# Kernel optimization log

Measured on AMD Instinct MI355X. Metric: run time of the kernel, lower is better.

## Reference

```python
import jax, jax.numpy as jnp
import numpy as np

N_NODES = 100000
N_EDGES = 1600000
IN_DIM = 64
OUT_DIM = 64
HIDDEN = 64  # fixed in edge_weight_mlp
POS_DIM = 3


def setup_inputs() -> dict:
    key = jax.random.key(0)
    ks = jax.random.split(key, 10)
    x = jax.random.normal(ks[0], (N_NODES, IN_DIM), dtype=jnp.float32)
    edge_index = jax.random.randint(ks[1], (2, N_EDGES), 0, N_NODES, dtype=jnp.int64)
    pos = jax.random.normal(ks[2], (N_NODES, POS_DIM), dtype=jnp.float32)
    # edge_weight_mlp params: Linear(2*IN_DIM+1 -> 64), Linear(64 -> 1)
    s1 = 1.0 / np.sqrt(2 * IN_DIM + 1)
    w1 = jax.random.uniform(ks[3], (2 * IN_DIM + 1, HIDDEN), jnp.float32, -s1, s1)
    b1 = jax.random.uniform(ks[4], (HIDDEN,), jnp.float32, -s1, s1)
    s2 = 1.0 / np.sqrt(HIDDEN)
    w2 = jax.random.uniform(ks[5], (HIDDEN, 1), jnp.float32, -s2, s2)
    b2 = jax.random.uniform(ks[6], (1,), jnp.float32, -s2, s2)
    # transform: Linear(IN_DIM -> OUT_DIM)
    st = 1.0 / np.sqrt(IN_DIM)
    wt = jax.random.uniform(ks[7], (IN_DIM, OUT_DIM), jnp.float32, -st, st)
    bt = jax.random.uniform(ks[8], (OUT_DIM,), jnp.float32, -st, st)
    return {"x": x, "edge_index": edge_index, "pos": pos,
            "w1": w1, "b1": b1, "w2": w2, "b2": b2, "wt": wt, "bt": bt}


def reference(x, edge_index, pos, w1, b1, w2, b2, wt, bt):
    src, dst = edge_index[0], edge_index[1]
    # edge weights: MLP on [x_src, x_dst, |pos_dst - pos_src|]
    edge_length = jnp.linalg.norm(pos[dst] - pos[src], axis=1, keepdims=True)  # [E,1]
    edge_feat = jnp.concatenate([x[src], x[dst], edge_length], axis=1)  # [E, 2*in+1]
    h = jax.nn.relu(edge_feat @ w1 + b1)
    edge_weights = jax.nn.sigmoid(h @ w2 + b2)  # [E,1]
    # node transform, gather, weight, scatter-add
    x_t = x @ wt + bt  # [N, out]
    messages = x_t[src] * edge_weights  # [E, out]
    out = jax.ops.segment_sum(messages, dst, num_segments=x.shape[0])  # [N, out]
    return out, edge_weights
```

## Files before the change

kernel.cpp:

```cpp
#include <hip/hip_runtime.h>
#include <hip/hip_bf16.h>
#include <math.h>

#define NN 100000
#define NE 1600000
#define CAP 48
#define NB 391
#define BCAP 4608
#define EPB 4096
#define NBLKA ((NE + EPB - 1) / EPB)
#define NPREP ((NN + 63) / 64)
#define PSTR 72

typedef __attribute__((ext_vector_type(8))) short short8;
typedef __attribute__((ext_vector_type(4))) float floatx4;
typedef __attribute__((ext_vector_type(2))) float float2v;

#if __has_builtin(__builtin_elementwise_fma)
#define VFMA(a, b, c) __builtin_elementwise_fma((a), (b), (c))
#else
#define VFMA(a, b, c) ((a) * (b) + (c))
#endif

static __device__ __forceinline__ unsigned short f2bb(float f) {
    __hip_bfloat16 h = __float2bfloat16(f);
    return *(unsigned short*)&h;
}
static __device__ __forceinline__ float hi_f(unsigned u) {
    return __uint_as_float(u & 0xFFFF0000u);
}
static __device__ __forceinline__ float lo_f(unsigned u) {
    return __uint_as_float(u << 16);
}
static __device__ __forceinline__ float2v hi2(unsigned a, unsigned b) {
    float2v r; r.x = __uint_as_float(a & 0xFFFF0000u);
    r.y = __uint_as_float(b & 0xFFFF0000u); return r;
}
static __device__ __forceinline__ float2v lo2(unsigned a, unsigned b) {
    float2v r; r.x = __uint_as_float(a << 16);
    r.y = __uint_as_float(b << 16); return r;
}

__global__ __launch_bounds__(256) void init_kernel(
    const float* __restrict__ w1, const float* __restrict__ wt,
    unsigned short* __restrict__ wb, int* __restrict__ gcursor) {
    int t = threadIdx.x;
    if (blockIdx.x == 0) {
        for (int i = t; i < NB; i += 256) gcursor[i] = 0;
    }
    int stride = gridDim.x * 256;
    for (int idx = blockIdx.x * 256 + t; idx < 192 * 64; idx += stride) {
        int n = idx >> 6;
        int k = idx & 63;
        float v = (n < 64)  ? w1[(size_t)k * 64 + n]
                : (n < 128) ? w1[(size_t)(64 + k) * 64 + (n - 64)]
                            : wt[(size_t)k * 64 + (n - 128)];
        wb[idx] = f2bb(v);
    }
}

__global__ __launch_bounds__(256) void fused_prep_bucket(
    const float* __restrict__ x, const unsigned short* __restrict__ wb,
    const float* __restrict__ b1, const float* __restrict__ pos,
    const int* __restrict__ ei,
    unsigned int* __restrict__ rec, unsigned short* __restrict__ hd,
    float4* __restrict__ pos4, int* __restrict__ gcursor,
    uint2* __restrict__ bucketed) {
    __shared__ __align__(16) unsigned char smem[(64 + 192) * PSTR * 2];
    int t = threadIdx.x;
    if (blockIdx.x < NPREP) {
        unsigned short* As = (unsigned short*)smem;
        unsigned short* Bs = As + 64 * PSTR;
        int nbase = blockIdx.x * 64;
        {
            int r = t & 63;
            int node = nbase + r; if (node >= NN) node = NN - 1;
            const float4* xr = (const float4*)(x + (size_t)node * 64);
#pragma unroll
            for (int i = 0; i < 4; ++i) {
                int s = (t >> 6) + 4 * i;
                float4 v = xr[s];
                ushort4 o = {f2bb(v.x), f2bb(v.y), f2bb(v.z), f2bb(v.w)};
                *(ushort4*)&As[r * PSTR + s * 4] = o;
            }
        }
        {
            const uint4* wb4 = (const uint4*)wb;
#pragma unroll
            for (int i = 0; i < 6; ++i) {
                int v = t + 256 * i;
                uint4 q = wb4[v];
                int n = v >> 3;
                int k = (v & 7) * 8;
                *(uint4*)&Bs[n * PSTR + k] = q;
            }
        }
        if (t < 64) {
            int node = nbase + t;
            if (node < NN)
                pos4[node] = make_float4(pos[node * 3 + 0], pos[node * 3 + 1],
                                         pos[node * 3 + 2], 0.f);
        }
        __syncthreads();
        int lane = t & 63, wave = t >> 6;
        int grp = lane >> 4, l15 = lane & 15;
        floatx4 acc[12] = {};
        int arow = wave * 16 + l15;
#pragma unroll
        for (int ks = 0; ks < 2; ++ks) {
            int koff = ks * 32 + grp * 8;
            short8 a = *(const short8*)&As[arow * PSTR + koff];
#pragma unroll
            for (int nt = 0; nt < 12; ++nt) {
                short8 b = *(const short8*)&Bs[(nt * 16 + l15) * PSTR + koff];
                acc[nt] = __builtin_amdgcn_mfma_f32_16x16x32_bf16(a, b, acc[nt], 0, 0, 0);
            }
        }
#pragma unroll
        for (int nt = 0; nt < 4; ++nt) {
#pragma unroll
            for (int r = 0; r < 4; ++r) {
                int nr = wave * 16 + grp * 4 + r;
                int node = nbase + nr;
                if (node >= NN) continue;
                int col = nt * 16 + l15;
                rec[(size_t)node * 64 + col] =
                    ((unsigned)f2bb(acc[nt][r]) << 16) | f2bb(acc[8 + nt][r]);
                hd[(size_t)node * 64 + col] = f2bb(acc[4 + nt][r] + b1[col]);
            }
        }
    } else {
        int* cnt = (int*)smem;
        int* base_s = cnt + NB;
        for (int i = t; i < NB; i += 256) cnt[i] = 0;
        __syncthreads();
        int e0 = (blockIdx.x - NPREP) * EPB;
        unsigned int tags[16];
        int srcs[16], dsts[16];
#pragma unroll
        for (int i = 0; i < 16; ++i) {
            int e = e0 + i * 256 + t;
            tags[i] = 0xFFFFFFFFu;
            if (e < NE) {
                srcs[i] = ei[e];
                dsts[i] = ei[NE + e];
                int b = dsts[i] >> 8;
                int slot = atomicAdd(&cnt[b], 1);
                tags[i] = ((unsigned)b << 12) | (unsigned)slot;
            }
        }
        __syncthreads();
        for (int b = t; b < NB; b += 256)
            base_s[b] = atomicAdd(&gcursor[b], cnt[b]);
        __syncthreads();
#pragma unroll
        for (int i = 0; i < 16; ++i) {
            if (tags[i] != 0xFFFFFFFFu) {
                int e = e0 + i * 256 + t;
                int b = (int)(tags[i] >> 12);
                int slot = (int)(tags[i] & 0xFFFu);
                int p = base_s[b] + slot;
                if (p < BCAP) {
                    bucketed[(size_t)b * BCAP + p] =
                        make_uint2((unsigned)srcs[i] |
                                   (((unsigned)dsts[i] & 255u) << 17),
                                   (unsigned)e);
                }
            }
        }
    }
}

__global__ __launch_bounds__(1024) void csr_kernel(
    const uint2* __restrict__ bucketed, const int* __restrict__ gcursor,
    uint2* __restrict__ pairs, int* __restrict__ deg) {
    __shared__ int cur[256];
    int t = threadIdx.x;
    if (t < 256) cur[t] = 0;
    __syncthreads();
    int b = blockIdx.x;
    int n0 = b << 8;
    int cnt = gcursor[b];
    if (cnt > BCAP) cnt = BCAP;
    for (int i = t; i < cnt; i += 1024) {
        uint2 en = bucketed[(size_t)b * BCAP + i];
        int dwb = (int)((en.x >> 17) & 255u);
        unsigned src = en.x & 0x1FFFFu;
        int slot = atomicAdd(&cur[dwb], 1);
        if (slot < CAP)
            pairs[(size_t)(n0 + dwb) * CAP + slot] = make_uint2(src, en.y);
    }
    __syncthreads();
    if (t < 256) {
        int node = n0 + t;
        if (node < NN) deg[node] = (cur[t] > CAP) ? CAP : cur[t];
    }
}

__global__ __launch_bounds__(256) void mega_kernel(
    const uint2* __restrict__ pairs, const int* __restrict__ deg,
    const unsigned int* __restrict__ rec, const unsigned short* __restrict__ hd,
    const float4* __restrict__ pos4, const float* __restrict__ w1,
    const float* __restrict__ w2, const float* __restrict__ b2,
    const float* __restrict__ bt,
    float* __restrict__ ew_out, float* __restrict__ out) {
    int t = threadIdx.x;
    int w = t >> 6, lane = t & 63;
    int e8 = lane >> 3, hg = lane & 7;
    int node = blockIdx.x * 4 + w;
    if (node >= NN) return;

    const float2v zero2 = {0.f, 0.f};
    float2v a01 = zero2, a23 = zero2, a45 = zero2, a67 = zero2;
    float sw = 0.f;
    int d = deg[node];
    uint4 hz = ((const uint4*)(hd + (size_t)node * 64))[hg];
    float2v zb01 = {lo_f(hz.x), hi_f(hz.x)};
    float2v zb23 = {lo_f(hz.y), hi_f(hz.y)};
    float2v zb45 = {lo_f(hz.z), hi_f(hz.z)};
    float2v zb67 = {lo_f(hz.w), hi_f(hz.w)};
    const float2v* w2p = (const float2v*)(w2 + 8 * hg);
    float2v w20 = w2p[0], w21 = w2p[1], w22 = w2p[2], w23 = w2p[3];
    const float2v* wlp = (const float2v*)(w1 + 128 * 64 + 8 * hg);
    float2v wl0 = wlp[0], wl1 = wlp[1], wl2 = wlp[2], wl3 = wlp[3];
    float4 bta = ((const float4*)bt)[2 * hg];
    float4 btb = ((const float4*)bt)[2 * hg + 1];
    float4 pd = pos4[node];
    float b2v = b2[0];
    const uint2* seg = pairs + (size_t)node * CAP;
    const uint4* rec4 = (const uint4*)rec;

    if (d > 0) {
        int i0 = (e8 < d) ? e8 : (d - 1);
        uint2 pr_c = seg[i0];
        uint2 pr_n = pr_c;
        if (8 < d) { int i1 = (8 + e8 < d) ? (8 + e8) : (d - 1); pr_n = seg[i1]; }
        uint4 ua_c = rec4[(size_t)pr_c.x * 16 + 2 * hg];
        uint4 ub_c = rec4[(size_t)pr_c.x * 16 + 2 * hg + 1];
        float4 ps_c = pos4[pr_c.x];

#pragma unroll 2
        for (int j = 0; j < d; j += 8) {
            int jn = j + 8;
            uint2 pr_n2 = pr_n;
            uint4 ua_n = ua_c, ub_n = ub_c;
            float4 ps_n = ps_c;
            if (jn < d) {
                ua_n = rec4[(size_t)pr_n.x * 16 + 2 * hg];
                ub_n = rec4[(size_t)pr_n.x * 16 + 2 * hg + 1];
                ps_n = pos4[pr_n.x];
                if (jn + 8 < d) {
                    int i2 = (jn + 8 + e8 < d) ? (jn + 8 + e8) : (d - 1);
                    pr_n2 = seg[i2];
                }
            }
            bool valid = (j + e8 < d);
            float dx = pd.x - ps_c.x;
            float dy = pd.y - ps_c.y;
            float dz = pd.z - ps_c.z;
            float len = __builtin_amdgcn_sqrtf(dx * dx + dy * dy + dz * dz);
            float2v l2; l2.x = len; l2.y = len;
            float2v z, r, tp;
            z = zb01 + hi2(ua_c.x, ua_c.y); z = VFMA(l2, wl0, z);
            r = __builtin_elementwise_max(z, zero2); tp = r * w20;
            z = zb23 + hi2(ua_c.z, ua_c.w); z = VFMA(l2, wl1, z);
            r = __builtin_elementwise_max(z, zero2); tp = VFMA(r, w21, tp);
            z = zb45 + hi2(ub_c.x, ub_c.y); z = VFMA(l2, wl2, z);
            r = __builtin_elementwise_max(z, zero2); tp = VFMA(r, w22, tp);
            z = zb67 + hi2(ub_c.z, ub_c.w); z = VFMA(l2, wl3, z);
            r = __builtin_elementwise_max(z, zero2); tp = VFMA(r, w23, tp);
            float tt = tp.x + tp.y;
            tt += __shfl_xor(tt, 1);
            tt += __shfl_xor(tt, 2);
            tt += __shfl_xor(tt, 4);
            float ew = __builtin_amdgcn_rcpf(1.f + __expf(-(tt + b2v)));
            if (valid) {
                if (hg == 0) ew_out[pr_c.y] = ew;
                float2v e2; e2.x = ew; e2.y = ew;
                a01 = VFMA(e2, lo2(ua_c.x, ua_c.y), a01);
                a23 = VFMA(e2, lo2(ua_c.z, ua_c.w), a23);
                a45 = VFMA(e2, lo2(ub_c.x, ub_c.y), a45);
                a67 = VFMA(e2, lo2(ub_c.z, ub_c.w), a67);
                sw += ew;
            }
            pr_c = pr_n; pr_n = pr_n2;
            ua_c = ua_n; ub_c = ub_n; ps_c = ps_n;
        }
    }
    float acc0 = a01.x, acc1 = a01.y, acc2 = a23.x, acc3 = a23.y;
    float acc4 = a45.x, acc5 = a45.y, acc6 = a67.x, acc7 = a67.y;
#pragma unroll
    for (int off = 8; off < 64; off <<= 1) {
        acc0 += __shfl_xor(acc0, off);
        acc1 += __shfl_xor(acc1, off);
        acc2 += __shfl_xor(acc2, off);
        acc3 += __shfl_xor(acc3, off);
        acc4 += __shfl_xor(acc4, off);
        acc5 += __shfl_xor(acc5, off);
        acc6 += __shfl_xor(acc6, off);
        acc7 += __shfl_xor(acc7, off);
        sw   += __shfl_xor(sw, off);
    }
    if (e8 == 0) {
        float* orow = out + (size_t)node * 64 + hg * 8;
        float4 o1 = {acc0 + sw * bta.x, acc1 + sw * bta.y,
                     acc2 + sw * bta.z, acc3 + sw * bta.w};
        float4 o2 = {acc4 + sw * btb.x, acc5 + sw * btb.y,
                     acc6 + sw * btb.z, acc7 + sw * btb.w};
        *(float4*)orow = o1;
        *(float4*)(orow + 4) = o2;
    }
}

extern "C" void kernel_launch(void* const* d_in, const int* in_sizes, int n_in,
                              void* d_out, int out_size, void* d_ws, size_t ws_size,
                              hipStream_t stream) {
    const float* x   = (const float*)d_in[0];
    const int*   ei  = (const int*)d_in[1];
    const float* pos = (const float*)d_in[2];
    const float* w1  = (const float*)d_in[3];
    const float* b1  = (const float*)d_in[4];
    const float* w2  = (const float*)d_in[5];
    const float* b2  = (const float*)d_in[6];
    const float* wt  = (const float*)d_in[7];
    const float* bt  = (const float*)d_in[8];

    float* out    = (float*)d_out;
    float* ew_out = out + (size_t)NN * 64;

    unsigned int* rec = (unsigned int*)d_ws;
    unsigned short* hd = (unsigned short*)(rec + (size_t)NN * 64);
    uint2* pairs = (uint2*)(hd + (size_t)NN * 64);
    float4* pos4 = (float4*)(pairs + (size_t)NN * CAP);
    int* gcursor = (int*)(pos4 + NN);
    int* deg = gcursor + NB;
    unsigned short* wb = (unsigned short*)(deg + NN);

    uint2* bucketed = (uint2*)d_out;

    init_kernel<<<16, 256, 0, stream>>>(w1, wt, wb, gcursor);
    fused_prep_bucket<<<NPREP + NBLKA, 256, 0, stream>>>(
        x, wb, b1, pos, ei, rec, hd, pos4, gcursor, bucketed);
    csr_kernel<<<NB, 1024, 0, stream>>>(bucketed, gcursor, pairs, deg);
    mega_kernel<<<(NN + 3) / 4, 256, 0, stream>>>(pairs, deg, rec, hd, pos4,
                                                  w1, w2, b2, bt, ew_out, out);
}
```

Before: 236.6 us.

## Stage bucketed edges in LDS via prefix scan for coalesced global writes

Both the bucketing pass and the CSR build now sort entries locally in shared memory using a block-wide prefix scan over bucket counts. They then write to global memory in contiguous runs instead of scattered per-entry stores. The aim is to cut uncoalesced scatter traffic in both passes. The cost is a larger LDS footprint, which may lower occupancy, plus extra scan steps and barriers. The per-thread register staging in csr_kernel assumes at most 5 entries per thread.

```diff
diff --git a/kernel.cpp b/kernel.cpp
--- a/kernel.cpp
+++ b/kernel.cpp
@@ -66,7 +66,7 @@
     unsigned int* __restrict__ rec, unsigned short* __restrict__ hd,
     float4* __restrict__ pos4, int* __restrict__ gcursor,
     uint2* __restrict__ bucketed) {
-    __shared__ __align__(16) unsigned char smem[(64 + 192) * PSTR * 2];
+    __shared__ __align__(16) unsigned char smem[40960];
     int t = threadIdx.x;
     if (blockIdx.x < NPREP) {
         unsigned short* As = (unsigned short*)smem;
@@ -130,9 +130,12 @@
             }
         }
     } else {
-        int* cnt = (int*)smem;
-        int* base_s = cnt + NB;
-        for (int i = t; i < NB; i += 256) cnt[i] = 0;
+        uint2* staged = (uint2*)smem;
+        int* cnt = (int*)(staged + EPB);
+        int* scA = cnt + 512;
+        int* scB = scA + 512;
+        int* base_s = scB + 512;
+        for (int i = t; i < 512; i += 256) cnt[i] = 0;
         __syncthreads();
         int e0 = (blockIdx.x - NPREP) * EPB;
         unsigned int tags[16];
@@ -150,23 +153,38 @@
             }
         }
         __syncthreads();
+        for (int i = t; i < 512; i += 256) scA[i] = cnt[i];
+        __syncthreads();
+        int* sp = scA; int* dp = scB;
+        for (int off = 1; off < 512; off <<= 1) {
+            for (int i = t; i < 512; i += 256)
+                dp[i] = sp[i] + ((i >= off) ? sp[i - off] : 0);
+            __syncthreads();
+            int* tmp = sp; sp = dp; dp = tmp;
+        }
         for (int b = t; b < NB; b += 256)
             base_s[b] = atomicAdd(&gcursor[b], cnt[b]);
-        __syncthreads();
 #pragma unroll
         for (int i = 0; i < 16; ++i) {
             if (tags[i] != 0xFFFFFFFFu) {
                 int e = e0 + i * 256 + t;
                 int b = (int)(tags[i] >> 12);
                 int slot = (int)(tags[i] & 0xFFFu);
-                int p = base_s[b] + slot;
-                if (p < BCAP) {
-                    bucketed[(size_t)b * BCAP + p] =
-                        make_uint2((unsigned)srcs[i] |
-                                   (((unsigned)dsts[i] & 255u) << 17),
-                                   (unsigned)e);
-                }
-            }
+                int pos = sp[b] - cnt[b] + slot;
+                staged[pos] = make_uint2(
+                    (unsigned)srcs[i] | (((unsigned)dsts[i] & 255u) << 17),
+                    (unsigned)e | ((unsigned)b << 21));
+            }
+        }
+        __syncthreads();
+        int total = sp[511];
+        for (int i = t; i < total; i += 256) {
+            uint2 en = staged[i];
+            int b = (int)(en.y >> 21);
+            int p = base_s[b] + (i - (sp[b] - cnt[b]));
+            if (p < BCAP)
+                bucketed[(size_t)b * BCAP + p] =
+                    make_uint2(en.x, en.y & 0x1FFFFFu);
         }
     }
 }
@@ -174,7 +192,8 @@
 __global__ __launch_bounds__(1024) void csr_kernel(
     const uint2* __restrict__ bucketed, const int* __restrict__ gcursor,
     uint2* __restrict__ pairs, int* __restrict__ deg) {
-    __shared__ int cur[256];
+    __shared__ uint2 staged[BCAP];
+    __shared__ int cur[256], scA[256], scB[256];
     int t = threadIdx.x;
     if (t < 256) cur[t] = 0;
     __syncthreads();
@@ -182,13 +201,41 @@
     int n0 = b << 8;
     int cnt = gcursor[b];
     if (cnt > BCAP) cnt = BCAP;
+    uint2 en_r[5];
+    int slot_r[5];
+    int k = 0;
     for (int i = t; i < cnt; i += 1024) {
         uint2 en = bucketed[(size_t)b * BCAP + i];
         int dwb = (int)((en.x >> 17) & 255u);
-        unsigned src = en.x & 0x1FFFFu;
-        int slot = atomicAdd(&cur[dwb], 1);
-        if (slot < CAP)
-            pairs[(size_t)(n0 + dwb) * CAP + slot] = make_uint2(src, en.y);
+        slot_r[k] = atomicAdd(&cur[dwb], 1);
+        en_r[k] = en;
+        ++k;
+    }
+    __syncthreads();
+    if (t < 256) scA[t] = cur[t];
+    __syncthreads();
+    int* sp = scA; int* dp = scB;
+    for (int off = 1; off < 256; off <<= 1) {
+        if (t < 256) dp[t] = sp[t] + ((t >= off) ? sp[t - off] : 0);
+        __syncthreads();
+        int* tmp = sp; sp = dp; dp = tmp;
+    }
+    k = 0;
+    for (int i = t; i < cnt; i += 1024) {
+        uint2 en = en_r[k];
+        int dwb = (int)((en.x >> 17) & 255u);
+        int pos = sp[dwb] - cur[dwb] + slot_r[k];
+        staged[pos] = en;
+        ++k;
+    }
+    __syncthreads();
+    for (int i = t; i < cnt; i += 1024) {
+        uint2 en = staged[i];
+        int dwb = (int)((en.x >> 17) & 255u);
+        int p = i - (sp[dwb] - cur[dwb]);
+        if (p < CAP)
+            pairs[(size_t)(n0 + dwb) * CAP + p] =
+                make_uint2(en.x & 0x1FFFFu, en.y);
     }
     __syncthreads();
     if (t < 256) {
```

After: 252.7 us. 6.8% more time.

## Fuse CSR build into gather kernel using LDS-staged per-bucket edge lists

Applied to the files above, without the earlier changes.

Removes the separate csr_kernel and its global pairs/deg arrays. Each 1024-thread block now loads its bucket of edges, counts per-destination slots with LDS atomics, prefix-sums the counts and scatters the edges into shared memory. The same block then runs the per-node edge MLP and aggregation from LDS, which saves a launch and a global write and read of the CSR. The cost is only NB=391 large blocks (about 37KB of LDS each), so fewer blocks run concurrently and there is less latency hiding for the gathers. The bucket buffer also moves from the output to the workspace, and the degree cap of 48 per node is gone.

```diff
diff --git a/kernel.cpp b/kernel.cpp
--- a/kernel.cpp
+++ b/kernel.cpp
@@ -4,7 +4,6 @@
 
 #define NN 100000
 #define NE 1600000
-#define CAP 48
 #define NB 391
 #define BCAP 4608
 #define EPB 4096
@@ -171,144 +170,157 @@
     }
 }
 
-__global__ __launch_bounds__(1024) void csr_kernel(
+__global__ __launch_bounds__(1024) void mega_kernel(
     const uint2* __restrict__ bucketed, const int* __restrict__ gcursor,
-    uint2* __restrict__ pairs, int* __restrict__ deg) {
-    __shared__ int cur[256];
-    int t = threadIdx.x;
-    if (t < 256) cur[t] = 0;
-    __syncthreads();
-    int b = blockIdx.x;
-    int n0 = b << 8;
-    int cnt = gcursor[b];
-    if (cnt > BCAP) cnt = BCAP;
-    for (int i = t; i < cnt; i += 1024) {
-        uint2 en = bucketed[(size_t)b * BCAP + i];
-        int dwb = (int)((en.x >> 17) & 255u);
-        unsigned src = en.x & 0x1FFFFu;
-        int slot = atomicAdd(&cur[dwb], 1);
-        if (slot < CAP)
-            pairs[(size_t)(n0 + dwb) * CAP + slot] = make_uint2(src, en.y);
-    }
-    __syncthreads();
-    if (t < 256) {
-        int node = n0 + t;
-        if (node < NN) deg[node] = (cur[t] > CAP) ? CAP : cur[t];
-    }
-}
-
-__global__ __launch_bounds__(256) void mega_kernel(
-    const uint2* __restrict__ pairs, const int* __restrict__ deg,
     const unsigned int* __restrict__ rec, const unsigned short* __restrict__ hd,
     const float4* __restrict__ pos4, const float* __restrict__ w1,
     const float* __restrict__ w2, const float* __restrict__ b2,
     const float* __restrict__ bt,
     float* __restrict__ ew_out, float* __restrict__ out) {
+    __shared__ uint2 staged[BCAP];
+    __shared__ int cur[256], scA[256], scB[256], off_s[256];
     int t = threadIdx.x;
+    int b = blockIdx.x;
+    int n0 = b << 8;
+    if (t < 256) cur[t] = 0;
+    __syncthreads();
+    int cnt = gcursor[b];
+    if (cnt > BCAP) cnt = BCAP;
+    uint2 en_r[5];
+    int slot_r[5];
+    int k = 0;
+    for (int i = t; i < cnt; i += 1024) {
+        uint2 en = bucketed[(size_t)b * BCAP + i];
+        int dwb = (int)((en.x >> 17) & 255u);
+        slot_r[k] = atomicAdd(&cur[dwb], 1);
+        en_r[k] = en;
+        ++k;
+    }
+    __syncthreads();
+    if (t < 256) scA[t] = cur[t];
+    __syncthreads();
+    int* sp = scA; int* dp = scB;
+    for (int off = 1; off < 256; off <<= 1) {
+        if (t < 256) dp[t] = sp[t] + ((t >= off) ? sp[t - off] : 0);
+        __syncthreads();
+        int* tmp = sp; sp = dp; dp = tmp;
+    }
+    if (t < 256) off_s[t] = sp[t] - cur[t];
+    __syncthreads();
+    k = 0;
+    for (int i = t; i < cnt; i += 1024) {
+        uint2 en = en_r[k];
+        int dwb = (int)((en.x >> 17) & 255u);
+        staged[off_s[dwb] + slot_r[k]] = en;
+        ++k;
+    }
+    __syncthreads();
+
     int w = t >> 6, lane = t & 63;
     int e8 = lane >> 3, hg = lane & 7;
-    int node = blockIdx.x * 4 + w;
-    if (node >= NN) return;
-
     const float2v zero2 = {0.f, 0.f};
-    float2v a01 = zero2, a23 = zero2, a45 = zero2, a67 = zero2;
-    float sw = 0.f;
-    int d = deg[node];
-    uint4 hz = ((const uint4*)(hd + (size_t)node * 64))[hg];
-    float2v zb01 = {lo_f(hz.x), hi_f(hz.x)};
-    float2v zb23 = {lo_f(hz.y), hi_f(hz.y)};
-    float2v zb45 = {lo_f(hz.z), hi_f(hz.z)};
-    float2v zb67 = {lo_f(hz.w), hi_f(hz.w)};
     const float2v* w2p = (const float2v*)(w2 + 8 * hg);
     float2v w20 = w2p[0], w21 = w2p[1], w22 = w2p[2], w23 = w2p[3];
     const float2v* wlp = (const float2v*)(w1 + 128 * 64 + 8 * hg);
     float2v wl0 = wlp[0], wl1 = wlp[1], wl2 = wlp[2], wl3 = wlp[3];
     float4 bta = ((const float4*)bt)[2 * hg];
     float4 btb = ((const float4*)bt)[2 * hg + 1];
-    float4 pd = pos4[node];
     float b2v = b2[0];
-    const uint2* seg = pairs + (size_t)node * CAP;
     const uint4* rec4 = (const uint4*)rec;
 
-    if (d > 0) {
-        int i0 = (e8 < d) ? e8 : (d - 1);
-        uint2 pr_c = seg[i0];
-        uint2 pr_n = pr_c;
-        if (8 < d) { int i1 = (8 + e8 < d) ? (8 + e8) : (d - 1); pr_n = seg[i1]; }
-        uint4 ua_c = rec4[(size_t)pr_c.x * 16 + 2 * hg];
-        uint4 ub_c = rec4[(size_t)pr_c.x * 16 + 2 * hg + 1];
-        float4 ps_c = pos4[pr_c.x];
+    for (int ni = 0; ni < 16; ++ni) {
+        int local = w * 16 + ni;
+        int node = n0 + local;
+        if (node >= NN) break;
+        float2v a01 = zero2, a23 = zero2, a45 = zero2, a67 = zero2;
+        float sw = 0.f;
+        int d = cur[local];
+        int so = off_s[local];
+        uint4 hz = ((const uint4*)(hd + (size_t)node * 64))[hg];
+        float2v zb01 = {lo_f(hz.x), hi_f(hz.x)};
+        float2v zb23 = {lo_f(hz.y), hi_f(hz.y)};
+        float2v zb45 = {lo_f(hz.z), hi_f(hz.z)};
+        float2v zb67 = {lo_f(hz.w), hi_f(hz.w)};
+        float4 pd = pos4[node];
+
+        if (d > 0) {
+            int i0 = (e8 < d) ? e8 : (d - 1);
+            uint2 pr_c = staged[so + i0];
+            unsigned s_c = pr_c.x & 0x1FFFFu;
+            uint4 ua_c = rec4[(size_t)s_c * 16 + 2 * hg];
+            uint4 ub_c = rec4[(size_t)s_c * 16 + 2 * hg + 1];
+            float4 ps_c = pos4[s_c];
 
 #pragma unroll 2
-        for (int j = 0; j < d; j += 8) {
-            int jn = j + 8;
-            uint2 pr_n2 = pr_n;
-            uint4 ua_n = ua_c, ub_n = ub_c;
-            float4 ps_n = ps_c;
-            if (jn < d) {
-                ua_n = rec4[(size_t)pr_n.x * 16 + 2 * hg];
-                ub_n = rec4[(size_t)pr_n.x * 16 + 2 * hg + 1];
-                ps_n = pos4[pr_n.x];
-                if (jn + 8 < d) {
-                    int i2 = (jn + 8 + e8 < d) ? (jn + 8 + e8) : (d - 1);
-                    pr_n2 = seg[i2];
+            for (int j = 0; j < d; j += 8) {
+                int jn = j + 8;
+                uint2 pr_n = pr_c;
+                uint4 ua_n = ua_c, ub_n = ub_c;
+                float4 ps_n = ps_c;
+                if (jn < d) {
+                    int i1 = (jn + e8 < d) ? (jn + e8) : (d - 1);
+                    pr_n = staged[so + i1];
+                    unsigned s_n = pr_n.x & 0x1FFFFu;
+                    ua_n = rec4[(size_t)s_n * 16 + 2 * hg];
+                    ub_n = rec4[(size_t)s_n * 16 + 2 * hg + 1];
+                    ps_n = pos4[s_n];
                 }
-            }
-            bool valid = (j + e8 < d);
-            float dx = pd.x - ps_c.x;
-            float dy = pd.y - ps_c.y;
-            float dz = pd.z - ps_c.z;
-            float len = __builtin_amdgcn_sqrtf(dx * dx + dy * dy + dz * dz);
-            float2v l2; l2.x = len; l2.y = len;
-            float2v z, r, tp;
-            z = zb01 + hi2(ua_c.x, ua_c.y); z = VFMA(l2, wl0, z);
-            r = __builtin_elementwise_max(z, zero2); tp = r * w20;
-            z = zb23 + hi2(ua_c.z, ua_c.w); z = VFMA(l2, wl1, z);
-            r = __builtin_elementwise_max(z, zero2); tp = VFMA(r, w21, tp);
-            z = zb45 + hi2(ub_c.x, ub_c.y); z = VFMA(l2, wl2, z);
-            r = __builtin_elementwise_max(z, zero2); tp = VFMA(r, w22, tp);
-            z = zb67 + hi2(ub_c.z, ub_c.w); z = VFMA(l2, wl3, z);
-            r = __builtin_elementwise_max(z, zero2); tp = VFMA(r, w23, tp);
-            float tt = tp.x + tp.y;
-            tt += __shfl_xor(tt, 1);
-            tt += __shfl_xor(tt, 2);
-            tt += __shfl_xor(tt, 4);
-            float ew = __builtin_amdgcn_rcpf(1.f + __expf(-(tt + b2v)));
-            if (valid) {
-                if (hg == 0) ew_out[pr_c.y] = ew;
-                float2v e2; e2.x = ew; e2.y = ew;
-                a01 = VFMA(e2, lo2(ua_c.x, ua_c.y), a01);
-                a23 = VFMA(e2, lo2(ua_c.z, ua_c.w), a23);
-                a45 = VFMA(e2, lo2(ub_c.x, ub_c.y), a45);
-                a67 = VFMA(e2, lo2(ub_c.z, ub_c.w), a67);
-                sw += ew;
-            }
-            pr_c = pr_n; pr_n = pr_n2;
-            ua_c = ua_n; ub_c = ub_n; ps_c = ps_n;
-        }
-    }
-    float acc0 = a01.x, acc1 = a01.y, acc2 = a23.x, acc3 = a23.y;
-    float acc4 = a45.x, acc5 = a45.y, acc6 = a67.x, acc7 = a67.y;
-#pragma unroll
-    for (int off = 8; off < 64; off <<= 1) {
-        acc0 += __shfl_xor(acc0, off);
-        acc1 += __shfl_xor(acc1, off);
-        acc2 += __shfl_xor(acc2, off);
-        acc3 += __shfl_xor(acc3, off);
-        acc4 += __shfl_xor(acc4, off);
-        acc5 += __shfl_xor(acc5, off);
-        acc6 += __shfl_xor(acc6, off);
-        acc7 += __shfl_xor(acc7, off);
-        sw   += __shfl_xor(sw, off);
-    }
-    if (e8 == 0) {
-        float* orow = out + (size_t)node * 64 + hg * 8;
-        float4 o1 = {acc0 + sw * bta.x, acc1 + sw * bta.y,
-                     acc2 + sw * bta.z, acc3 + sw * bta.w};
-        float4 o2 = {acc4 + sw * btb.x, acc5 + sw * btb.y,
-                     acc6 + sw * btb.z, acc7 + sw * btb.w};
-        *(float4*)orow = o1;
-        *(float4*)(orow + 4) = o2;
+                bool valid = (j + e8 < d);
+                float dx = pd.x - ps_c.x;
+                float dy = pd.y - ps_c.y;
+                float dz = pd.z - ps_c.z;
+                float len = __builtin_amdgcn_sqrtf(dx * dx + dy * dy + dz * dz);
+                float2v l2; l2.x = len; l2.y = len;
+                float2v z, r, tp;
+                z = zb01 + hi2(ua_c.x, ua_c.y); z = VFMA(l2, wl0, z);
+                r = __builtin_elementwise_max(z, zero2); tp = r * w20;
+                z = zb23 + hi2(ua_c.z, ua_c.w); z = VFMA(l2, wl1, z);
+                r = __builtin_elementwise_max(z, zero2); tp = VFMA(r, w21, tp);
+                z = zb45 + hi2(ub_c.x, ub_c.y); z = VFMA(l2, wl2, z);
+                r = __builtin_elementwise_max(z, zero2); tp = VFMA(r, w22, tp);
+                z = zb67 + hi2(ub_c.z, ub_c.w); z = VFMA(l2, wl3, z);
+                r = __builtin_elementwise_max(z, zero2); tp = VFMA(r, w23, tp);
+                float tt = tp.x + tp.y;
+                tt += __shfl_xor(tt, 1);
+                tt += __shfl_xor(tt, 2);
+                tt += __shfl_xor(tt, 4);
+                float ew = __builtin_amdgcn_rcpf(1.f + __expf(-(tt + b2v)));
+                if (valid) {
+                    if (hg == 0) ew_out[pr_c.y] = ew;
+                    float2v e2; e2.x = ew; e2.y = ew;
+                    a01 = VFMA(e2, lo2(ua_c.x, ua_c.y), a01);
+                    a23 = VFMA(e2, lo2(ua_c.z, ua_c.w), a23);
+                    a45 = VFMA(e2, lo2(ub_c.x, ub_c.y), a45);
+                    a67 = VFMA(e2, lo2(ub_c.z, ub_c.w), a67);
+                    sw += ew;
+                }
+                pr_c = pr_n;
+                ua_c = ua_n; ub_c = ub_n; ps_c = ps_n;
+            }
+        }
+        float acc0 = a01.x, acc1 = a01.y, acc2 = a23.x, acc3 = a23.y;
+        float acc4 = a45.x, acc5 = a45.y, acc6 = a67.x, acc7 = a67.y;
+#pragma unroll
+        for (int off = 8; off < 64; off <<= 1) {
+            acc0 += __shfl_xor(acc0, off);
+            acc1 += __shfl_xor(acc1, off);
+            acc2 += __shfl_xor(acc2, off);
+            acc3 += __shfl_xor(acc3, off);
+            acc4 += __shfl_xor(acc4, off);
+            acc5 += __shfl_xor(acc5, off);
+            acc6 += __shfl_xor(acc6, off);
+            acc7 += __shfl_xor(acc7, off);
+            sw   += __shfl_xor(sw, off);
+        }
+        if (e8 == 0) {
+            float* orow = out + (size_t)node * 64 + hg * 8;
+            float4 o1 = {acc0 + sw * bta.x, acc1 + sw * bta.y,
+                         acc2 + sw * bta.z, acc3 + sw * bta.w};
+            float4 o2 = {acc4 + sw * btb.x, acc5 + sw * btb.y,
+                         acc6 + sw * btb.z, acc7 + sw * btb.w};
+            *(float4*)orow = o1;
+            *(float4*)(orow + 4) = o2;
+        }
     }
 }
 
@@ -330,18 +342,14 @@
 
     unsigned int* rec = (unsigned int*)d_ws;
     unsigned short* hd = (unsigned short*)(rec + (size_t)NN * 64);
-    uint2* pairs = (uint2*)(hd + (size_t)NN * 64);
-    float4* pos4 = (float4*)(pairs + (size_t)NN * CAP);
+    uint2* bucketed = (uint2*)(hd + (size_t)NN * 64);
+    float4* pos4 = (float4*)(bucketed + (size_t)NB * BCAP);
     int* gcursor = (int*)(pos4 + NN);
-    int* deg = gcursor + NB;
-    unsigned short* wb = (unsigned short*)(deg + NN);
-
-    uint2* bucketed = (uint2*)d_out;
+    unsigned short* wb = (unsigned short*)(gcursor + NB);
 
     init_kernel<<<16, 256, 0, stream>>>(w1, wt, wb, gcursor);
     fused_prep_bucket<<<NPREP + NBLKA, 256, 0, stream>>>(
         x, wb, b1, pos, ei, rec, hd, pos4, gcursor, bucketed);
-    csr_kernel<<<NB, 1024, 0, stream>>>(bucketed, gcursor, pairs, deg);
-    mega_kernel<<<(NN + 3) / 4, 256, 0, stream>>>(pairs, deg, rec, hd, pos4,
-                                                  w1, w2, b2, bt, ew_out, out);
-}
+    mega_kernel<<<NB, 1024, 0, stream>>>(bucketed, gcursor, rec, hd, pos4,
+                                         w1, w2, b2, bt, ew_out, out);
+}
```

Measured after the change: 250.9 us. 6.0% more time.

## Split fused prep/bucket kernel into separate launches with larger prep tiles

Applied to the files above, without the earlier changes.

Undoes the fusion of node-transform GEMM blocks and edge-bucketing blocks into one launch, and issues them as two kernels on the same stream. The prep kernel now uses 512 threads covering 128 nodes per block, which halves the number of times each block stages the weight matrix into shared memory. It also uses packed bf16 conversion instructions and hoists the bias load out of the inner loop. The cost is one extra kernel launch and the loss of any overlap between the two heterogeneous block types.

```diff
diff --git a/kernel.cpp b/kernel.cpp
--- a/kernel.cpp
+++ b/kernel.cpp
@@ -9,7 +9,7 @@
 #define BCAP 4608
 #define EPB 4096
 #define NBLKA ((NE + EPB - 1) / EPB)
-#define NPREP ((NN + 63) / 64)
+#define NPREP2 ((NN + 127) / 128)
 #define PSTR 72
 
 typedef __attribute__((ext_vector_type(8))) short short8;
@@ -25,6 +25,11 @@
 static __device__ __forceinline__ unsigned short f2bb(float f) {
     __hip_bfloat16 h = __float2bfloat16(f);
     return *(unsigned short*)&h;
+}
+static __device__ __forceinline__ unsigned cvt_pk_bf16(float lo, float hi) {
+    unsigned r;
+    asm("v_cvt_pk_bf16_f32 %0, %1, %2" : "=v"(r) : "v"(lo), "v"(hi));
+    return r;
 }
 static __device__ __forceinline__ float hi_f(unsigned u) {
     return __uint_as_float(u & 0xFFFF0000u);
@@ -59,113 +64,114 @@
     }
 }
 
-__global__ __launch_bounds__(256) void fused_prep_bucket(
+__global__ __launch_bounds__(512) void prep_kernel(
     const float* __restrict__ x, const unsigned short* __restrict__ wb,
     const float* __restrict__ b1, const float* __restrict__ pos,
-    const int* __restrict__ ei,
     unsigned int* __restrict__ rec, unsigned short* __restrict__ hd,
-    float4* __restrict__ pos4, int* __restrict__ gcursor,
+    float4* __restrict__ pos4) {
+    __shared__ __align__(16) unsigned short As[128 * PSTR];
+    __shared__ __align__(16) unsigned short Bs[192 * PSTR];
+    int t = threadIdx.x;
+    int nbase = blockIdx.x * 128;
+    {
+        int r = t & 127;
+        int node = nbase + r; if (node >= NN) node = NN - 1;
+        const float4* xr = (const float4*)(x + (size_t)node * 64);
+#pragma unroll
+        for (int i = 0; i < 4; ++i) {
+            int s = (t >> 7) + 4 * i;
+            float4 v = xr[s];
+            *(uint2*)&As[r * PSTR + s * 4] =
+                make_uint2(cvt_pk_bf16(v.x, v.y), cvt_pk_bf16(v.z, v.w));
+        }
+    }
+    {
+        const uint4* wb4 = (const uint4*)wb;
+#pragma unroll
+        for (int i = 0; i < 3; ++i) {
+            int v = t + 512 * i;
+            uint4 q = wb4[v];
+            int n = v >> 3;
+            int k = (v & 7) * 8;
+            *(uint4*)&Bs[n * PSTR + k] = q;
+        }
+    }
+    if (t < 128) {
+        int node = nbase + t;
+        if (node < NN)
+            pos4[node] = make_float4(pos[node * 3 + 0], pos[node * 3 + 1],
+                                     pos[node * 3 + 2], 0.f);
+    }
+    __syncthreads();
+    int lane = t & 63, wave = t >> 6;
+    int grp = lane >> 4, l15 = lane & 15;
+    floatx4 acc[12] = {};
+    int arow = wave * 16 + l15;
+#pragma unroll
+    for (int ks = 0; ks < 2; ++ks) {
+        int koff = ks * 32 + grp * 8;
+        short8 a = *(const short8*)&As[arow * PSTR + koff];
+#pragma unroll
+        for (int nt = 0; nt < 12; ++nt) {
+            short8 b = *(const short8*)&Bs[(nt * 16 + l15) * PSTR + koff];
+            acc[nt] = __builtin_amdgcn_mfma_f32_16x16x32_bf16(a, b, acc[nt], 0, 0, 0);
+        }
+    }
+#pragma unroll
+    for (int nt = 0; nt < 4; ++nt) {
+        int col = nt * 16 + l15;
+        float b1v = b1[col];
+#pragma unroll
+        for (int r = 0; r < 4; ++r) {
+            int nr = wave * 16 + grp * 4 + r;
+            int node = nbase + nr;
+            if (node >= NN) continue;
+            rec[(size_t)node * 64 + col] =
+                cvt_pk_bf16(acc[8 + nt][r], acc[nt][r]);
+            hd[(size_t)node * 64 + col] = f2bb(acc[4 + nt][r] + b1v);
+        }
+    }
+}
+
+__global__ __launch_bounds__(256) void bucket_kernel(
+    const int* __restrict__ ei, int* __restrict__ gcursor,
     uint2* __restrict__ bucketed) {
-    __shared__ __align__(16) unsigned char smem[(64 + 192) * PSTR * 2];
-    int t = threadIdx.x;
-    if (blockIdx.x < NPREP) {
-        unsigned short* As = (unsigned short*)smem;
-        unsigned short* Bs = As + 64 * PSTR;
-        int nbase = blockIdx.x * 64;
-        {
-            int r = t & 63;
-            int node = nbase + r; if (node >= NN) node = NN - 1;
-            const float4* xr = (const float4*)(x + (size_t)node * 64);
-#pragma unroll
-            for (int i = 0; i < 4; ++i) {
-                int s = (t >> 6) + 4 * i;
-                float4 v = xr[s];
-                ushort4 o = {f2bb(v.x), f2bb(v.y), f2bb(v.z), f2bb(v.w)};
-                *(ushort4*)&As[r * PSTR + s * 4] = o;
-            }
-        }
-        {
-            const uint4* wb4 = (const uint4*)wb;
-#pragma unroll
-            for (int i = 0; i < 6; ++i) {
-                int v = t + 256 * i;
-                uint4 q = wb4[v];
-                int n = v >> 3;
-                int k = (v & 7) * 8;
-                *(uint4*)&Bs[n * PSTR + k] = q;
-            }
-        }
-        if (t < 64) {
-            int node = nbase + t;
-            if (node < NN)
-                pos4[node] = make_float4(pos[node * 3 + 0], pos[node * 3 + 1],
-                                         pos[node * 3 + 2], 0.f);
-        }
-        __syncthreads();
-        int lane = t & 63, wave = t >> 6;
-        int grp = lane >> 4, l15 = lane & 15;
-        floatx4 acc[12] = {};
-        int arow = wave * 16 + l15;
-#pragma unroll
-        for (int ks = 0; ks < 2; ++ks) {
-            int koff = ks * 32 + grp * 8;
-            short8 a = *(const short8*)&As[arow * PSTR + koff];
-#pragma unroll
-            for (int nt = 0; nt < 12; ++nt) {
-                short8 b = *(const short8*)&Bs[(nt * 16 + l15) * PSTR + koff];
-                acc[nt] = __builtin_amdgcn_mfma_f32_16x16x32_bf16(a, b, acc[nt], 0, 0, 0);
-            }
-        }
-#pragma unroll
-        for (int nt = 0; nt < 4; ++nt) {
-#pragma unroll
-            for (int r = 0; r < 4; ++r) {
-                int nr = wave * 16 + grp * 4 + r;
-                int node = nbase + nr;
-                if (node >= NN) continue;
-                int col = nt * 16 + l15;
-                rec[(size_t)node * 64 + col] =
-                    ((unsigned)f2bb(acc[nt][r]) << 16) | f2bb(acc[8 + nt][r]);
-                hd[(size_t)node * 64 + col] = f2bb(acc[4 + nt][r] + b1[col]);
-            }
-        }
-    } else {
-        int* cnt = (int*)smem;
-        int* base_s = cnt + NB;
-        for (int i = t; i < NB; i += 256) cnt[i] = 0;
-        __syncthreads();
-        int e0 = (blockIdx.x - NPREP) * EPB;
-        unsigned int tags[16];
-        int srcs[16], dsts[16];
-#pragma unroll
-        for (int i = 0; i < 16; ++i) {
+    __shared__ int cnt[NB];
+    __shared__ int base_s[NB];
+    int t = threadIdx.x;
+    for (int i = t; i < NB; i += 256) cnt[i] = 0;
+    __syncthreads();
+    int e0 = blockIdx.x * EPB;
+    unsigned int tags[16];
+    int srcs[16], dsts[16];
+#pragma unroll
+    for (int i = 0; i < 16; ++i) {
+        int e = e0 + i * 256 + t;
+        tags[i] = 0xFFFFFFFFu;
+        if (e < NE) {
+            srcs[i] = ei[e];
+            dsts[i] = ei[NE + e];
+            int b = dsts[i] >> 8;
+            int slot = atomicAdd(&cnt[b], 1);
+            tags[i] = ((unsigned)b << 12) | (unsigned)slot;
+        }
+    }
+    __syncthreads();
+    for (int b = t; b < NB; b += 256)
+        base_s[b] = atomicAdd(&gcursor[b], cnt[b]);
+    __syncthreads();
+#pragma unroll
+    for (int i = 0; i < 16; ++i) {
+        if (tags[i] != 0xFFFFFFFFu) {
             int e = e0 + i * 256 + t;
-            tags[i] = 0xFFFFFFFFu;
-            if (e < NE) {
-                srcs[i] = ei[e];
-                dsts[i] = ei[NE + e];
-                int b = dsts[i] >> 8;
-                int slot = atomicAdd(&cnt[b], 1);
-                tags[i] = ((unsigned)b << 12) | (unsigned)slot;
-            }
-        }
-        __syncthreads();
-        for (int b = t; b < NB; b += 256)
-            base_s[b] = atomicAdd(&gcursor[b], cnt[b]);
-        __syncthreads();
-#pragma unroll
-        for (int i = 0; i < 16; ++i) {
-            if (tags[i] != 0xFFFFFFFFu) {
-                int e = e0 + i * 256 + t;
-                int b = (int)(tags[i] >> 12);
-                int slot = (int)(tags[i] & 0xFFFu);
-                int p = base_s[b] + slot;
-                if (p < BCAP) {
-                    bucketed[(size_t)b * BCAP + p] =
-                        make_uint2((unsigned)srcs[i] |
-                                   (((unsigned)dsts[i] & 255u) << 17),
-                                   (unsigned)e);
-                }
+            int b = (int)(tags[i] >> 12);
+            int slot = (int)(tags[i] & 0xFFFu);
+            int p = base_s[b] + slot;
+            if (p < BCAP) {
+                bucketed[(size_t)b * BCAP + p] =
+                    make_uint2((unsigned)srcs[i] |
+                               (((unsigned)dsts[i] & 255u) << 17),
+                               (unsigned)e);
             }
         }
     }
@@ -339,8 +345,8 @@
     uint2* bucketed = (uint2*)d_out;
 
     init_kernel<<<16, 256, 0, stream>>>(w1, wt, wb, gcursor);
-    fused_prep_bucket<<<NPREP + NBLKA, 256, 0, stream>>>(
-        x, wb, b1, pos, ei, rec, hd, pos4, gcursor, bucketed);
+    bucket_kernel<<<NBLKA, 256, 0, stream>>>(ei, gcursor, bucketed);
+    prep_kernel<<<NPREP2, 512, 0, stream>>>(x, wb, b1, pos, rec, hd, pos4);
     csr_kernel<<<NB, 1024, 0, stream>>>(bucketed, gcursor, pairs, deg);
     mega_kernel<<<(NN + 3) / 4, 256, 0, stream>>>(pairs, deg, rec, hd, pos4,
                                                   w1, w2, b2, bt, ew_out, out);
```

New measurement: 242.1 us. +2.3%, slower.
